# Kernel tuning notes

Measured on AMD Instinct MI355X. Metric: run time of the kernel, lower is better.

The kernel has to match this reference:

```python
import jax, jax.numpy as jnp
import numpy as np

BN_EPS = 1e-5
N_OUT, D_OUT = 64, 128


def setup_inputs() -> dict:
    key = jax.random.key(0)
    k1, k2, k3, k4 = jax.random.split(key, 4)
    B, N_in, D_in, K = 512, 64, 128, 4
    x = jax.random.normal(k1, (B, N_in, D_in), dtype=jnp.float32)
    # block-sparse weights: one (D_in x D_out) block per (output-row, active-input-row) pair
    W = jax.random.normal(k2, (N_OUT, K, D_in, D_OUT), dtype=jnp.float32) * (1.0 / np.sqrt(K * D_in))
    bias = jax.random.normal(k3, (N_OUT, D_OUT), dtype=jnp.float32) * 0.02
    gamma = jnp.ones((N_OUT * D_OUT,), dtype=jnp.float32)
    beta = jnp.zeros((N_OUT * D_OUT,), dtype=jnp.float32)
    idx = jax.random.randint(k4, (N_OUT, K), 0, N_in, dtype=jnp.int32)
    return {"x": x, "W": W, "bias": bias, "gamma": gamma, "beta": beta, "idx": idx}


def reference(x, W, bias, gamma, beta, idx):
    B = x.shape[0]
    # structured-sparse linear: gather active input rows, per-block matmul
    xg = x[:, idx, :]                                   # [B, N_out, K, D_in]
    y = jnp.einsum('bokd,okde->boe', xg, W) + bias      # [B, N_out, D_out]
    # BatchNorm1d (training-mode batch statistics) on flattened features
    yf = y.reshape(B, -1)                               # [B, N_out*D_out]
    mean = jnp.mean(yf, axis=0)
    var = jnp.mean(jnp.square(yf - mean), axis=0)       # biased variance, as in torch BN
    yn = (yf - mean) * jax.lax.rsqrt(var + BN_EPS) * gamma + beta
    # Swish: z * sigmoid(z)
    out = yn * jax.nn.sigmoid(yn)
    return out.reshape(B, N_OUT, D_OUT)
```

## Files before the change

### kernel.cpp

```cpp
#include <hip/hip_runtime.h>


typedef __attribute__((ext_vector_type(8))) __bf16 bf16x8;
typedef __attribute__((ext_vector_type(4))) float  f32x4;

#define FEAT 8192
#define XROWP 8320
#define LDSB 520
#define NX8  524288
#define ADEPTH 6

__global__ __launch_bounds__(256)
void cvt_kernel(const float* __restrict__ x, __bf16* __restrict__ xb)
{
    const int stride = gridDim.x * blockDim.x;
    for (int c = blockIdx.x * blockDim.x + threadIdx.x; c < NX8; c += stride) {
        const int b = c >> 10;
        const int j = c & 1023;
        const f32x4 v0 = *(const f32x4*)(x + c * 8);
        const f32x4 v1 = *(const f32x4*)(x + c * 8 + 4);
        bf16x8 o;
#pragma unroll
        for (int jj = 0; jj < 4; ++jj) {
            o[jj]     = (__bf16)v0[jj];
            o[jj + 4] = (__bf16)v1[jj];
        }
        *(bf16x8*)(xb + (size_t)b * XROWP + j * 8) = o;
    }
}

__global__ __launch_bounds__(1024, 4)
void fused_encoder(const __bf16* __restrict__ xb, const float* __restrict__ W,
                   const float* __restrict__ bias, const float* __restrict__ gamma,
                   const float* __restrict__ beta, const int* __restrict__ idxp,
                   float* __restrict__ out)
{
    __shared__ __bf16 Bpan[32 * LDSB];
    __shared__ float Sred[16][32];
    __shared__ float Qred[16][32];
    __shared__ float sscale[32];
    __shared__ float sshift[32];

    const int bid = blockIdx.x;
    const int o   = ((bid >> 5) << 3) | (bid & 7);
    const int es  = (bid >> 3) & 3;
    const int e0  = es * 32;

    const int tid  = threadIdx.x;
    const int wave = tid >> 6;
    const int lane = tid & 63;
    const int lam  = lane & 15;
    const int quad = lane >> 4;

    const int r0 = idxp[o * 4 + 0];
    const int r1 = idxp[o * 4 + 1];
    const int r2 = idxp[o * 4 + 2];
    const int r3 = idxp[o * 4 + 3];

    const __bf16* xrow0 = xb + (size_t)(wave * 32 + lam)      * XROWP;
    const __bf16* xrow1 = xb + (size_t)(wave * 32 + 16 + lam) * XROWP;

    auto rowOf = [&](const int kc) -> int {
        const int kidx = kc >> 2;
        const int ra = (kidx & 1) ? r1 : r0;
        const int rb = (kidx & 1) ? r3 : r2;
        return (kidx & 2) ? rb : ra;
    };

    bf16x8 sa[ADEPTH][2];
    auto loadA = [&](bf16x8& F0, bf16x8& F1, const int kc) {
        const int r  = rowOf(kc);
        const int dd = (kc & 3) * 32 + quad * 8;
        F0 = *(const bf16x8*)(xrow0 + r * 128 + dd);
        F1 = *(const bf16x8*)(xrow1 + r * 128 + dd);
    };

    const int kk0 = wave;

#pragma unroll
    for (int p = 0; p < ADEPTH; ++p)
        loadA(sa[p][0], sa[p][1], (kk0 + p) & 15);

    {
        const int e  = tid & 31;
        const int k0 = (tid >> 5) * 16;
        float v[16];
#pragma unroll
        for (int j = 0; j < 16; ++j) {
            const int k = k0 + j;
            v[j] = W[(((o * 4 + (k >> 7)) * 128) + (k & 127)) * 128 + e0 + e];
        }
        bf16x8 w0, w1;
#pragma unroll
        for (int j = 0; j < 8; ++j) {
            w0[j] = (__bf16)v[j];
            w1[j] = (__bf16)v[8 + j];
        }
        *(bf16x8*)&Bpan[e * LDSB + k0]     = w0;
        *(bf16x8*)&Bpan[e * LDSB + k0 + 8] = w1;
    }

    const f32x4 zero4 = {0.f, 0.f, 0.f, 0.f};
    f32x4 acc[2][2];
#pragma unroll
    for (int mi = 0; mi < 2; ++mi)
#pragma unroll
        for (int ni = 0; ni < 2; ++ni) acc[mi][ni] = zero4;

    __syncthreads();

    bf16x8 bq[2][2];
    bq[0][0] = *(const bf16x8*)&Bpan[lam        * LDSB + kk0 * 32 + quad * 8];
    bq[0][1] = *(const bf16x8*)&Bpan[(16 + lam) * LDSB + kk0 * 32 + quad * 8];

#pragma unroll
    for (int i = 0; i < 16; ++i) {
        const int cur = i & 1;
        const int stg = i % ADEPTH;
        if (i + 1 < 16) {
            const int kn = (kk0 + i + 1) & 15;
            bq[cur ^ 1][0] = *(const bf16x8*)&Bpan[lam        * LDSB + kn * 32 + quad * 8];
            bq[cur ^ 1][1] = *(const bf16x8*)&Bpan[(16 + lam) * LDSB + kn * 32 + quad * 8];
        }
        acc[0][0] = __builtin_amdgcn_mfma_f32_16x16x32_bf16(sa[stg][0], bq[cur][0], acc[0][0], 0, 0, 0);
        acc[0][1] = __builtin_amdgcn_mfma_f32_16x16x32_bf16(sa[stg][0], bq[cur][1], acc[0][1], 0, 0, 0);
        acc[1][0] = __builtin_amdgcn_mfma_f32_16x16x32_bf16(sa[stg][1], bq[cur][0], acc[1][0], 0, 0, 0);
        acc[1][1] = __builtin_amdgcn_mfma_f32_16x16x32_bf16(sa[stg][1], bq[cur][1], acc[1][1], 0, 0, 0);
        if (i + ADEPTH < 16)
            loadA(sa[stg][0], sa[stg][1], (kk0 + i + ADEPTH) & 15);
    }

    float bvals[2];
#pragma unroll
    for (int ni = 0; ni < 2; ++ni)
        bvals[ni] = bias[o * 128 + e0 + ni * 16 + lam];
#pragma unroll
    for (int mi = 0; mi < 2; ++mi)
#pragma unroll
        for (int ni = 0; ni < 2; ++ni)
#pragma unroll
            for (int rr = 0; rr < 4; ++rr) acc[mi][ni][rr] += bvals[ni];

#pragma unroll
    for (int ni = 0; ni < 2; ++ni) {
        float s = 0.f, q = 0.f;
#pragma unroll
        for (int mi = 0; mi < 2; ++mi)
#pragma unroll
            for (int rr = 0; rr < 4; ++rr) {
                const float v = acc[mi][ni][rr];
                s += v; q += v * v;
            }
        s += __shfl_xor(s, 16); s += __shfl_xor(s, 32);
        q += __shfl_xor(q, 16); q += __shfl_xor(q, 32);
        if (quad == 0) {
            Sred[wave][ni * 16 + lam] = s;
            Qred[wave][ni * 16 + lam] = q;
        }
    }
    __syncthreads();

    if (tid < 32) {
        float s = 0.f, q = 0.f;
#pragma unroll
        for (int w = 0; w < 16; ++w) {
            s += Sred[w][tid];
            q += Qred[w][tid];
        }
        const float mean = s * (1.0f / 512.0f);
        const float var  = q * (1.0f / 512.0f) - mean * mean;
        const float rstd = rsqrtf(var + 1e-5f);
        const float sc   = rstd * gamma[o * 128 + e0 + tid];
        sscale[tid] = sc;
        sshift[tid] = beta[o * 128 + e0 + tid] - mean * sc;
    }
    __syncthreads();

#pragma unroll
    for (int mi = 0; mi < 2; ++mi) {
        const int rowb = wave * 32 + mi * 16 + quad * 4;
#pragma unroll
        for (int ni = 0; ni < 2; ++ni) {
            const int col = ni * 16 + lam;
            const float sc = sscale[col];
            const float sh = sshift[col];
#pragma unroll
            for (int rr = 0; rr < 4; ++rr) {
                const float xn = acc[mi][ni][rr] * sc + sh;
                const float sg = 1.0f / (1.0f + __expf(-xn));
                out[(rowb + rr) * FEAT + o * 128 + e0 + col] = xn * sg;
            }
        }
    }
}

extern "C" void kernel_launch(void* const* d_in, const int* in_sizes, int n_in,
                              void* d_out, int out_size, void* d_ws, size_t ws_size,
                              hipStream_t stream)
{
    const float* x     = (const float*)d_in[0];
    const float* W     = (const float*)d_in[1];
    const float* bias  = (const float*)d_in[2];
    const float* gamma = (const float*)d_in[3];
    const float* beta  = (const float*)d_in[4];
    const int*   idx   = (const int*)d_in[5];
    float* out = (float*)d_out;

    __bf16* xb = (__bf16*)d_ws;

    cvt_kernel<<<dim3(512), dim3(256), 0, stream>>>(x, xb);
    fused_encoder<<<dim3(256), dim3(1024), 0, stream>>>(
        xb, W, bias, gamma, beta, idx, out);
}
```

Before: 105.9 us.

## Halve block to 512 threads with 64-row-per-wave MFMA tiles

Each block now uses 8 waves instead of 16, and each wave covers 64 batch rows (four 16-row M tiles) instead of 32. Each B fragment read from LDS is therefore reused across four MFMAs, halving LDS reads per MFMA. The 6-deep A prefetch is replaced by a 2-stage double buffer of four fragments per stage, so less global-load latency is hidden. Fewer waves per block lowers latency hiding, and the W panel staging loads 32 values per thread instead of 16, which raises register pressure.

```diff
diff --git a/kernel.cpp b/kernel.cpp
--- a/kernel.cpp
+++ b/kernel.cpp
@@ -8,7 +8,6 @@
 #define XROWP 8320
 #define LDSB 520
 #define NX8  524288
-#define ADEPTH 6
 
 __global__ __launch_bounds__(256)
 void cvt_kernel(const float* __restrict__ x, __bf16* __restrict__ xb)
@@ -29,15 +28,15 @@
     }
 }
 
-__global__ __launch_bounds__(1024, 4)
+__global__ __launch_bounds__(512, 4)
 void fused_encoder(const __bf16* __restrict__ xb, const float* __restrict__ W,
                    const float* __restrict__ bias, const float* __restrict__ gamma,
                    const float* __restrict__ beta, const int* __restrict__ idxp,
                    float* __restrict__ out)
 {
     __shared__ __bf16 Bpan[32 * LDSB];
-    __shared__ float Sred[16][32];
-    __shared__ float Qred[16][32];
+    __shared__ float Sred[8][32];
+    __shared__ float Qred[8][32];
     __shared__ float sscale[32];
     __shared__ float sshift[32];
 
@@ -56,9 +55,6 @@
     const int r1 = idxp[o * 4 + 1];
     const int r2 = idxp[o * 4 + 2];
     const int r3 = idxp[o * 4 + 3];
-
-    const __bf16* xrow0 = xb + (size_t)(wave * 32 + lam)      * XROWP;
-    const __bf16* xrow1 = xb + (size_t)(wave * 32 + 16 + lam) * XROWP;
 
     auto rowOf = [&](const int kc) -> int {
         const int kidx = kc >> 2;
@@ -67,67 +63,83 @@
         return (kidx & 2) ? rb : ra;
     };
 
-    bf16x8 sa[ADEPTH][2];
-    auto loadA = [&](bf16x8& F0, bf16x8& F1, const int kc) {
-        const int r  = rowOf(kc);
-        const int dd = (kc & 3) * 32 + quad * 8;
-        F0 = *(const bf16x8*)(xrow0 + r * 128 + dd);
-        F1 = *(const bf16x8*)(xrow1 + r * 128 + dd);
+    const __bf16* xr0 = xb + (size_t)(wave * 64 +  0 + lam) * XROWP;
+    const __bf16* xr1 = xb + (size_t)(wave * 64 + 16 + lam) * XROWP;
+    const __bf16* xr2 = xb + (size_t)(wave * 64 + 32 + lam) * XROWP;
+    const __bf16* xr3 = xb + (size_t)(wave * 64 + 48 + lam) * XROWP;
+
+    bf16x8 sa0[4], sa1[4];
+    auto loadA = [&](bf16x8 (&S)[4], const int kc) {
+        const int r   = rowOf(kc);
+        const int off = r * 128 + (kc & 3) * 32 + quad * 8;
+        S[0] = *(const bf16x8*)(xr0 + off);
+        S[1] = *(const bf16x8*)(xr1 + off);
+        S[2] = *(const bf16x8*)(xr2 + off);
+        S[3] = *(const bf16x8*)(xr3 + off);
     };
 
-    const int kk0 = wave;
-
-#pragma unroll
-    for (int p = 0; p < ADEPTH; ++p)
-        loadA(sa[p][0], sa[p][1], (kk0 + p) & 15);
+    const int kk0 = wave * 2;
+    loadA(sa0, kk0 & 15);
+    loadA(sa1, (kk0 + 1) & 15);
 
     {
         const int e  = tid & 31;
-        const int k0 = (tid >> 5) * 16;
-        float v[16];
-#pragma unroll
-        for (int j = 0; j < 16; ++j) {
+        const int k0 = (tid >> 5) * 32;
+        float v[32];
+#pragma unroll
+        for (int j = 0; j < 32; ++j) {
             const int k = k0 + j;
             v[j] = W[(((o * 4 + (k >> 7)) * 128) + (k & 127)) * 128 + e0 + e];
         }
-        bf16x8 w0, w1;
-#pragma unroll
-        for (int j = 0; j < 8; ++j) {
-            w0[j] = (__bf16)v[j];
-            w1[j] = (__bf16)v[8 + j];
-        }
-        *(bf16x8*)&Bpan[e * LDSB + k0]     = w0;
-        *(bf16x8*)&Bpan[e * LDSB + k0 + 8] = w1;
+#pragma unroll
+        for (int c = 0; c < 4; ++c) {
+            bf16x8 w;
+#pragma unroll
+            for (int j = 0; j < 8; ++j) w[j] = (__bf16)v[c * 8 + j];
+            *(bf16x8*)&Bpan[e * LDSB + k0 + c * 8] = w;
+        }
     }
 
     const f32x4 zero4 = {0.f, 0.f, 0.f, 0.f};
-    f32x4 acc[2][2];
-#pragma unroll
-    for (int mi = 0; mi < 2; ++mi)
+    f32x4 acc[4][2];
+#pragma unroll
+    for (int mi = 0; mi < 4; ++mi)
 #pragma unroll
         for (int ni = 0; ni < 2; ++ni) acc[mi][ni] = zero4;
 
     __syncthreads();
 
-    bf16x8 bq[2][2];
-    bq[0][0] = *(const bf16x8*)&Bpan[lam        * LDSB + kk0 * 32 + quad * 8];
-    bq[0][1] = *(const bf16x8*)&Bpan[(16 + lam) * LDSB + kk0 * 32 + quad * 8];
+    bf16x8 bq0[2], bq1[2];
+    bq0[0] = *(const bf16x8*)&Bpan[lam        * LDSB + kk0 * 32 + quad * 8];
+    bq0[1] = *(const bf16x8*)&Bpan[(16 + lam) * LDSB + kk0 * 32 + quad * 8];
 
 #pragma unroll
     for (int i = 0; i < 16; ++i) {
-        const int cur = i & 1;
-        const int stg = i % ADEPTH;
-        if (i + 1 < 16) {
-            const int kn = (kk0 + i + 1) & 15;
-            bq[cur ^ 1][0] = *(const bf16x8*)&Bpan[lam        * LDSB + kn * 32 + quad * 8];
-            bq[cur ^ 1][1] = *(const bf16x8*)&Bpan[(16 + lam) * LDSB + kn * 32 + quad * 8];
-        }
-        acc[0][0] = __builtin_amdgcn_mfma_f32_16x16x32_bf16(sa[stg][0], bq[cur][0], acc[0][0], 0, 0, 0);
-        acc[0][1] = __builtin_amdgcn_mfma_f32_16x16x32_bf16(sa[stg][0], bq[cur][1], acc[0][1], 0, 0, 0);
-        acc[1][0] = __builtin_amdgcn_mfma_f32_16x16x32_bf16(sa[stg][1], bq[cur][0], acc[1][0], 0, 0, 0);
-        acc[1][1] = __builtin_amdgcn_mfma_f32_16x16x32_bf16(sa[stg][1], bq[cur][1], acc[1][1], 0, 0, 0);
-        if (i + ADEPTH < 16)
-            loadA(sa[stg][0], sa[stg][1], (kk0 + i + ADEPTH) & 15);
+        if ((i & 1) == 0) {
+            if (i + 1 < 16) {
+                const int kn = (kk0 + i + 1) & 15;
+                bq1[0] = *(const bf16x8*)&Bpan[lam        * LDSB + kn * 32 + quad * 8];
+                bq1[1] = *(const bf16x8*)&Bpan[(16 + lam) * LDSB + kn * 32 + quad * 8];
+            }
+#pragma unroll
+            for (int mi = 0; mi < 4; ++mi) {
+                acc[mi][0] = __builtin_amdgcn_mfma_f32_16x16x32_bf16(sa0[mi], bq0[0], acc[mi][0], 0, 0, 0);
+                acc[mi][1] = __builtin_amdgcn_mfma_f32_16x16x32_bf16(sa0[mi], bq0[1], acc[mi][1], 0, 0, 0);
+            }
+            if (i + 2 < 16) loadA(sa0, (kk0 + i + 2) & 15);
+        } else {
+            if (i + 1 < 16) {
+                const int kn = (kk0 + i + 1) & 15;
+                bq0[0] = *(const bf16x8*)&Bpan[lam        * LDSB + kn * 32 + quad * 8];
+                bq0[1] = *(const bf16x8*)&Bpan[(16 + lam) * LDSB + kn * 32 + quad * 8];
+            }
+#pragma unroll
+            for (int mi = 0; mi < 4; ++mi) {
+                acc[mi][0] = __builtin_amdgcn_mfma_f32_16x16x32_bf16(sa1[mi], bq1[0], acc[mi][0], 0, 0, 0);
+                acc[mi][1] = __builtin_amdgcn_mfma_f32_16x16x32_bf16(sa1[mi], bq1[1], acc[mi][1], 0, 0, 0);
+            }
+            if (i + 2 < 16) loadA(sa1, (kk0 + i + 2) & 15);
+        }
     }
 
     float bvals[2];
@@ -135,7 +147,7 @@
     for (int ni = 0; ni < 2; ++ni)
         bvals[ni] = bias[o * 128 + e0 + ni * 16 + lam];
 #pragma unroll
-    for (int mi = 0; mi < 2; ++mi)
+    for (int mi = 0; mi < 4; ++mi)
 #pragma unroll
         for (int ni = 0; ni < 2; ++ni)
 #pragma unroll
@@ -145,7 +157,7 @@
     for (int ni = 0; ni < 2; ++ni) {
         float s = 0.f, q = 0.f;
 #pragma unroll
-        for (int mi = 0; mi < 2; ++mi)
+        for (int mi = 0; mi < 4; ++mi)
 #pragma unroll
             for (int rr = 0; rr < 4; ++rr) {
                 const float v = acc[mi][ni][rr];
@@ -163,7 +175,7 @@
     if (tid < 32) {
         float s = 0.f, q = 0.f;
 #pragma unroll
-        for (int w = 0; w < 16; ++w) {
+        for (int w = 0; w < 8; ++w) {
             s += Sred[w][tid];
             q += Qred[w][tid];
         }
@@ -177,8 +189,8 @@
     __syncthreads();
 
 #pragma unroll
-    for (int mi = 0; mi < 2; ++mi) {
-        const int rowb = wave * 32 + mi * 16 + quad * 4;
+    for (int mi = 0; mi < 4; ++mi) {
+        const int rowb = wave * 64 + mi * 16 + quad * 4;
 #pragma unroll
         for (int ni = 0; ni < 2; ++ni) {
             const int col = ni * 16 + lam;
@@ -209,6 +221,6 @@
     __bf16* xb = (__bf16*)d_ws;
 
     cvt_kernel<<<dim3(512), dim3(256), 0, stream>>>(x, xb);
-    fused_encoder<<<dim3(256), dim3(1024), 0, stream>>>(
+    fused_encoder<<<dim3(256), dim3(512), 0, stream>>>(
         xb, W, bias, gamma, beta, idx, out);
 }
```

Result: no change. 106.4 us (+0.6%).
